# Performance work log

Measured on AMD Instinct MI355X. Metric: run time of the kernel, lower is better.

The kernel has to match this reference:

```python
import jax, jax.numpy as jnp
import numpy as np

G = 16  # grid (window) size, fixed in the module


def _ln_channels(x, w, b, eps=1e-5):
    # LayerNorm4D: normalize over channel dim of NCHW
    mu = x.mean(axis=1, keepdims=True)
    var = ((x - mu) ** 2).mean(axis=1, keepdims=True)
    return (x - mu) / jnp.sqrt(var + eps) * w[None, :, None, None] + b[None, :, None, None]


def setup_inputs() -> dict:
    key = jax.random.key(0)
    ks = jax.random.split(key, 8)
    B, C, H, W = 8, 256, 128, 128
    C8, F = C // 8, 4 * C
    s = 0.02
    return {
        "x": jax.random.normal(ks[0], (B, C, H, W), jnp.float32),
        "Wq": jax.random.normal(ks[1], (C8, C), jnp.float32) * s,
        "Wk": jax.random.normal(ks[2], (C8, C), jnp.float32) * s,
        "Wv": jax.random.normal(ks[3], (C, C), jnp.float32) * s,
        "gamma": jnp.float32(1.0),
        "W1": jax.random.normal(ks[4], (F, C), jnp.float32) * s,
        "b1": jnp.zeros((F,), jnp.float32),
        "W2": jax.random.normal(ks[5], (C, F), jnp.float32) * s,
        "b2": jnp.zeros((C,), jnp.float32),
        "ln1_w": jnp.ones((C,), jnp.float32),
        "ln1_b": jnp.zeros((C,), jnp.float32),
        "ln2_w": jnp.ones((C,), jnp.float32),
        "ln2_b": jnp.zeros((C,), jnp.float32),
    }


def reference(x, Wq, Wk, Wv, gamma, W1, b1, W2, b2, ln1_w, ln1_b, ln2_w, ln2_b):
    B, C, H, W = x.shape
    nh, nw = H // G, W // G
    N = G * G  # tokens per window
    # gather all 16x16 windows into the batch dim: [B*nh*nw, C, N]
    xw = x.reshape(B, C, nh, G, nw, G).transpose(0, 2, 4, 1, 3, 5).reshape(B * nh * nw, C, N)
    # SAGAN-style self-attention within each window
    q = jnp.einsum('oc,bcn->bno', Wq, xw)                 # [Bw, N, C/8]
    k = jnp.einsum('oc,bcn->bon', Wk, xw)                 # [Bw, C/8, N]
    attn = jax.nn.softmax(jnp.einsum('bno,bom->bnm', q, k), axis=-1)  # [Bw, N, N]
    v = jnp.einsum('oc,bcn->bon', Wv, xw)                 # [Bw, C, N]
    out = jnp.einsum('bcn,bmn->bcm', v, attn)             # v @ attn^T
    aw = gamma * out + xw
    # scatter windows back to NCHW
    xa = aw.reshape(B, nh, nw, C, G, G).transpose(0, 3, 1, 4, 2, 5).reshape(B, C, H, W)
    # FFN: 1x1 conv -> GELU(exact) -> 1x1 conv (dropout is identity in eval)
    h1 = jax.nn.gelu(jnp.einsum('fc,bchw->bfhw', W1, xa) + b1[None, :, None, None], approximate=False)
    y = jnp.einsum('cf,bfhw->bchw', W2, h1) + b2[None, :, None, None]
    x2 = xa + _ln_channels(y, ln1_w, ln1_b)
    return x2 + _ln_channels(x2, ln2_w, ln2_b)
```

## Files before the change

### kernel.cpp

```cpp
#include <hip/hip_runtime.h>
#include <hip/hip_bf16.h>

#define C_DIM 256
#define HW_DIM 16384
#define F_DIM 1024

typedef __hip_bfloat16 bf16;
typedef short short8 __attribute__((ext_vector_type(8)));
typedef float f32x4 __attribute__((ext_vector_type(4)));

__device__ __forceinline__ float bf2f(unsigned short u) {
  unsigned int x = ((unsigned int)u) << 16;
  return __uint_as_float(x);
}
__device__ __forceinline__ unsigned short f2bfbits(float v) {
  bf16 h = __float2bfloat16(v);
  return *(unsigned short*)&h;
}


__global__ __launch_bounds__(256) void prep_weights(
    const float* __restrict__ Wq, const float* __restrict__ Wk,
    const float* __restrict__ Wv, const float* __restrict__ W1,
    const float* __restrict__ W2, unsigned short* __restrict__ Wqkv,
    unsigned short* __restrict__ W1s, unsigned short* __restrict__ W2s) {
  int i = blockIdx.x * 256 + threadIdx.x;
  if (i < 320 * 256) {
    int r = i >> 8, c = i & 255;
    float v;
    if (r < 32)      v = Wq[r * 256 + c];
    else if (r < 64) v = Wk[(r - 32) * 256 + c];
    else             v = Wv[(r - 64) * 256 + c];
    Wqkv[i] = f2bfbits(v);
  }
  if (i < 32768) {
    int ft = i >> 9, ks = (i >> 6) & 7, l = i & 63;
    int f = ft * 16 + (l & 15), kb = ks * 32 + (l >> 4) * 8;
    #pragma unroll
    for (int j = 0; j < 8; ++j)
      W1s[i * 8 + j] = f2bfbits(W1[f * 256 + kb + j]);
  }
  if (i < 32768) {
    int ct = i >> 11, gks = (i >> 6) & 31, l = i & 63;
    int c = ct * 16 + (l & 15), fb = gks * 32 + (l >> 4) * 8;
    #pragma unroll
    for (int j = 0; j < 8; ++j)
      W2s[i * 8 + j] = f2bfbits(W2[c * 1024 + fb + j]);
  }
}

__global__ __launch_bounds__(256) void xprep_kernel(
    const float* __restrict__ x, unsigned short* __restrict__ Xfrag) {
  const int gtid = blockIdx.x * 256 + threadIdx.x;
  const int win = gtid >> 13;
  const int rem = gtid & 8191;
  const int mt = rem >> 9, ks = (rem >> 6) & 7, l = rem & 63;
  const int t = l & 15, q = l >> 4;
  const int b = win >> 6, wh = (win >> 3) & 7, ww = win & 7;
  const int h = wh * 16 + mt, w = ww * 16 + t;
  const int c0 = ks * 32 + q * 8;
  const float* xp = x + ((size_t)(b * 256 + c0) * 128 + h) * 128 + w;
  short8 v;
  #pragma unroll
  for (int j = 0; j < 8; ++j)
    v[j] = (short)f2bfbits(xp[(size_t)j * 16384]);
  *(short8*)(Xfrag + (size_t)gtid * 8) = v;
}

__global__ __launch_bounds__(256) void qkvproj_kernel(
    const unsigned short* __restrict__ Xfrag, const unsigned short* __restrict__ Wqkv,
    unsigned short* __restrict__ Qw, unsigned short* __restrict__ Kw,
    unsigned short* __restrict__ Vw) {
  const int bid = blockIdx.x;
  const int win = bid >> 2, mc = bid & 3;
  const int m0 = mc * 64;
  const int tid = threadIdx.x;
  const int wv = tid >> 6, l = tid & 63;
  const int t = l & 15, q = l >> 4;
  const unsigned short* Xb = Xfrag + (size_t)win * 65536;

  for (int mt = 0; mt < 4; ++mt) {
    short8 Bf[8];
    #pragma unroll
    for (int ks = 0; ks < 8; ++ks)
      Bf[ks] = *(const short8*)(Xb + (((size_t)(mc * 4 + mt) * 8 + ks) * 64 + l) * 8);
    #pragma unroll
    for (int rti = 0; rti < 5; ++rti) {
      const int rt = wv * 5 + rti;
      const int r0 = rt * 16;
      f32x4 acc = (f32x4){0.f, 0.f, 0.f, 0.f};
      #pragma unroll
      for (int ks = 0; ks < 8; ++ks) {
        short8 av = *(const short8*)(Wqkv + (size_t)(r0 + t) * 256 + ks * 32 + q * 8);
        acc = __builtin_amdgcn_mfma_f32_16x16x32_bf16(av, Bf[ks], acc, 0, 0, 0);
      }
      const int n = m0 + mt * 16 + t;
      if (rt < 4) {
        ushort4 u;
        u.x = f2bfbits(acc[0]); u.y = f2bfbits(acc[1]);
        u.z = f2bfbits(acc[2]); u.w = f2bfbits(acc[3]);
        unsigned short* dst = (rt < 2) ? Qw : Kw;
        int o0 = (rt & 1) * 16 + q * 4;
        *(ushort4*)(dst + ((size_t)win * 256 + n) * 32 + o0) = u;
      } else {
        #pragma unroll
        for (int r = 0; r < 4; ++r) {
          int c = r0 - 64 + q * 4 + r;
          Vw[((size_t)win * 256 + c) * 256 + n] = f2bfbits(acc[r]);
        }
      }
    }
  }
}

__global__ __launch_bounds__(256, 4) void attn_fused_kernel(
    const unsigned short* __restrict__ Qw, const unsigned short* __restrict__ Kw,
    const unsigned short* __restrict__ Vw, const unsigned short* __restrict__ Xfrag,
    const float* __restrict__ gamma, unsigned short* __restrict__ XAfrag) {
  __shared__ __align__(16) short Ps[2][64][72];
  __shared__ float Lpart[4][64];
  __shared__ float Ls[64];

  const int bid = blockIdx.x;
  const int wgb = (bid & 7) * 256 + (bid >> 3);
  const int win = wgb >> 2, wr = wgb & 3;

  const int tid = threadIdx.x;
  const int wc = tid >> 6, l = tid & 63;
  const int t = l & 15, q = l >> 4;

  f32x4 Oacc[4][4];
  #pragma unroll
  for (int k = 0; k < 4; ++k)
    #pragma unroll
    for (int i = 0; i < 4; ++i)
      Oacc[k][i] = (f32x4){0.f, 0.f, 0.f, 0.f};
  float lsum[16];
  #pragma unroll
  for (int e = 0; e < 16; ++e) lsum[e] = 0.f;

  const unsigned short* Qb = Qw + (size_t)win * 256 * 32;
  const unsigned short* Kb = Kw + (size_t)win * 256 * 32;
  const unsigned short* Vb = Vw + (size_t)win * 65536;

  short8 aq[4];
  #pragma unroll
  for (int i = 0; i < 4; ++i)
    aq[i] = *(const short8*)(Qb + (size_t)((wr * 4 + i) * 16 + t) * 32 + q * 8);

  for (int mcc = 0; mcc < 4; ++mcc) {
    const int buf = mcc & 1;
    {
      const int m0s = (mcc * 4 + wc) * 16;
      short8 bk = *(const short8*)(Kb + (size_t)(m0s + t) * 32 + q * 8);
      f32x4 sv[4];
      #pragma unroll
      for (int i = 0; i < 4; ++i)
        sv[i] = __builtin_amdgcn_mfma_f32_16x16x32_bf16(aq[i], bk, (f32x4){0.f,0.f,0.f,0.f}, 0, 0, 0);
      #pragma unroll
      for (int i = 0; i < 4; ++i) {
        #pragma unroll
        for (int r = 0; r < 4; ++r) {
          float e = __expf(sv[i][r]);
          lsum[i * 4 + r] += e;
          Ps[buf][i * 16 + q * 4 + r][wc * 16 + t] = (short)f2bfbits(e);
        }
      }
    }
    __syncthreads();
    #pragma unroll
    for (int ks2 = 0; ks2 < 2; ++ks2) {
      short8 ap[4], bv[4];
      #pragma unroll
      for (int i = 0; i < 4; ++i)
        ap[i] = *(const short8*)&Ps[buf][i * 16 + t][ks2 * 32 + q * 8];
      #pragma unroll
      for (int k = 0; k < 4; ++k)
        bv[k] = *(const short8*)(Vb + (size_t)((wc * 4 + k) * 16 + t) * 256 + mcc * 64 + ks2 * 32 + q * 8);
      #pragma unroll
      for (int k = 0; k < 4; ++k)
        #pragma unroll
        for (int i = 0; i < 4; ++i)
          Oacc[k][i] = __builtin_amdgcn_mfma_f32_16x16x32_bf16(bv[k], ap[i], Oacc[k][i], 0, 0, 0);
    }
  }

  #pragma unroll
  for (int mask = 1; mask < 16; mask <<= 1)
    #pragma unroll
    for (int e = 0; e < 16; ++e)
      lsum[e] += __shfl_xor(lsum[e], mask);
  __syncthreads();
  if (t == 0) {
    #pragma unroll
    for (int i = 0; i < 4; ++i)
      *(float4*)&Lpart[wc][i * 16 + q * 4] =
          make_float4(lsum[i * 4 + 0], lsum[i * 4 + 1], lsum[i * 4 + 2], lsum[i * 4 + 3]);
  }
  __syncthreads();
  if (tid < 64) {
    float s = Lpart[0][tid] + Lpart[1][tid] + Lpart[2][tid] + Lpart[3][tid];
    Ls[tid] = gamma[0] / s;
  }
  __syncthreads();

  const unsigned short* Xres = Xfrag + (size_t)win * 65536;
  unsigned short* XAb = XAfrag + (size_t)win * 65536;
  #pragma unroll
  for (int i = 0; i < 4; ++i) {
    const float ls = Ls[i * 16 + t];
    #pragma unroll
    for (int k = 0; k < 4; ++k) {
      const size_t off = (((size_t)(wr * 4 + i) * 8 + wc * 2 + (k >> 1)) * 64 +
                          ((k & 1) * 2 + (q >> 1)) * 16 + t) * 8 + (q & 1) * 4;
      ushort4 xa4 = *(const ushort4*)(Xres + off);
      const unsigned short* xp = (const unsigned short*)&xa4;
      ushort4 u;
      unsigned short* up = (unsigned short*)&u;
      #pragma unroll
      for (int r = 0; r < 4; ++r)
        up[r] = f2bfbits(ls * Oacc[k][i][r] + bf2f(xp[r]));
      *(ushort4*)(XAb + off) = u;
    }
  }
}

__global__ __launch_bounds__(256, 3) void ffn_mfma_kernel(
    const unsigned short* __restrict__ XAfrag,
    const unsigned short* __restrict__ W1s, const unsigned short* __restrict__ W2s,
    const float* __restrict__ b1, const float* __restrict__ b2,
    const float* __restrict__ ln1w, const float* __restrict__ ln1b,
    const float* __restrict__ ln2w, const float* __restrict__ ln2b,
    float* __restrict__ out) {
  __shared__ __align__(16) short Xf[4][8][64][8];
  __shared__ __align__(16) short Ht[64][136];
  __shared__ float red[2][4][64];

  const int bid = blockIdx.x;
  const int win = bid >> 2, mc = bid & 3;
  const int b = win >> 6, wh = (win >> 3) & 7, ww = win & 7;
  const int tid = threadIdx.x;
  const int wv = tid >> 6, l = tid & 63;
  const int p = l & 15, q = l >> 4;
  const unsigned short* XAb = XAfrag + (size_t)win * 65536 + (size_t)mc * 16384;

  {
    const short8* src = (const short8*)XAb;
    short8* dst = (short8*)&Xf[0][0][0][0];
    #pragma unroll
    for (int rep = 0; rep < 8; ++rep)
      dst[rep * 256 + tid] = src[rep * 256 + tid];
  }
  __syncthreads();

  f32x4 Yacc[4][4];
  #pragma unroll
  for (int i = 0; i < 4; ++i)
    #pragma unroll
    for (int pt = 0; pt < 4; ++pt)
      Yacc[i][pt] = (f32x4){0.f, 0.f, 0.f, 0.f};

  const short8* W1s8 = (const short8*)W1s;
  const short8* W2s8 = (const short8*)W2s;

  for (int fc = 0; fc < 8; ++fc) {
    f32x4 Hacc[2][4];
    #pragma unroll
    for (int i = 0; i < 2; ++i)
      #pragma unroll
      for (int pt = 0; pt < 4; ++pt)
        Hacc[i][pt] = (f32x4){0.f, 0.f, 0.f, 0.f};
    const int f0 = (fc * 8 + wv * 2) * 8;
    #pragma unroll
    for (int ks = 0; ks < 8; ++ks) {
      short8 a0 = W1s8[(f0 + ks) * 64 + l];
      short8 a1 = W1s8[(f0 + 8 + ks) * 64 + l];
      #pragma unroll
      for (int pt = 0; pt < 4; ++pt) {
        short8 bf = *(const short8*)&Xf[pt][ks][l][0];
        Hacc[0][pt] = __builtin_amdgcn_mfma_f32_16x16x32_bf16(a0, bf, Hacc[0][pt], 0, 0, 0);
        Hacc[1][pt] = __builtin_amdgcn_mfma_f32_16x16x32_bf16(a1, bf, Hacc[1][pt], 0, 0, 0);
      }
    }
    __syncthreads();
    #pragma unroll
    for (int i = 0; i < 2; ++i) {
      float4 bv1 = *(const float4*)(b1 + fc * 128 + wv * 32 + i * 16 + q * 4);
      #pragma unroll
      for (int pt = 0; pt < 4; ++pt) {
        ushort4 hbv;
        unsigned short* hp = (unsigned short*)&hbv;
        #pragma unroll
        for (int r = 0; r < 4; ++r) {
          float v = Hacc[i][pt][r] + ((const float*)&bv1)[r];
          float u = 0.7978845608f * fmaf(0.044715f * v, v * v, v);
          float e = __expf(2.f * u);
          float g = v - v / (e + 1.f);
          hp[r] = f2bfbits(g);
        }
        *(ushort4*)&Ht[pt * 16 + p][wv * 32 + i * 16 + q * 4] = hbv;
      }
    }
    __syncthreads();
    #pragma unroll
    for (int fs = 0; fs < 4; ++fs) {
      short8 av[4];
      #pragma unroll
      for (int i = 0; i < 4; ++i)
        av[i] = W2s8[((wv * 4 + i) * 32 + fc * 4 + fs) * 64 + l];
      #pragma unroll
      for (int pt = 0; pt < 4; ++pt) {
        short8 bf = *(const short8*)&Ht[pt * 16 + p][fs * 32 + q * 8];
        #pragma unroll
        for (int i = 0; i < 4; ++i)
          Yacc[i][pt] = __builtin_amdgcn_mfma_f32_16x16x32_bf16(av[i], bf, Yacc[i][pt], 0, 0, 0);
      }
    }
  }

  #pragma unroll
  for (int i = 0; i < 4; ++i) {
    float4 bb = *(const float4*)(b2 + wv * 64 + i * 16 + q * 4);
    #pragma unroll
    for (int pt = 0; pt < 4; ++pt)
      #pragma unroll
      for (int r = 0; r < 4; ++r)
        Yacc[i][pt][r] += ((const float*)&bb)[r];
  }

  #pragma unroll
  for (int pt = 0; pt < 4; ++pt) {
    float ss = 0.f, sq = 0.f;
    #pragma unroll
    for (int i = 0; i < 4; ++i)
      #pragma unroll
      for (int r = 0; r < 4; ++r) { float v = Yacc[i][pt][r]; ss += v; sq += v * v; }
    ss += __shfl_xor(ss, 16); sq += __shfl_xor(sq, 16);
    ss += __shfl_xor(ss, 32); sq += __shfl_xor(sq, 32);
    if (l < 16) { red[0][wv][pt * 16 + l] = ss; red[1][wv][pt * 16 + l] = sq; }
  }
  __syncthreads();
  if (tid < 64) {
    float S  = red[0][0][tid] + red[0][1][tid] + red[0][2][tid] + red[0][3][tid];
    float Q2 = red[1][0][tid] + red[1][1][tid] + red[1][2][tid] + red[1][3][tid];
    float m = S * 0.00390625f;
    float va = Q2 * 0.00390625f - m * m;
    red[0][0][tid] = m; red[1][0][tid] = rsqrtf(va + 1e-5f);
  }
  __syncthreads();
  #pragma unroll
  for (int i = 0; i < 4; ++i) {
    float4 w1v = *(const float4*)(ln1w + wv * 64 + i * 16 + q * 4);
    float4 b1v = *(const float4*)(ln1b + wv * 64 + i * 16 + q * 4);
    const int ksx = wv * 2 + (i >> 1);
    const int lq = (i & 1) * 2 + (q >> 1);
    #pragma unroll
    for (int pt = 0; pt < 4; ++pt) {
      int px = pt * 16 + p;
      float mu = red[0][0][px], rs = red[1][0][px];
      ushort4 xa4 = *(const ushort4*)&Xf[pt][ksx][lq * 16 + p][(q & 1) * 4];
      const unsigned short* xp = (const unsigned short*)&xa4;
      #pragma unroll
      for (int r = 0; r < 4; ++r)
        Yacc[i][pt][r] = bf2f(xp[r]) + (Yacc[i][pt][r] - mu) * rs * ((const float*)&w1v)[r] + ((const float*)&b1v)[r];
    }
  }
  __syncthreads();
  #pragma unroll
  for (int pt = 0; pt < 4; ++pt) {
    float ss = 0.f, sq = 0.f;
    #pragma unroll
    for (int i = 0; i < 4; ++i)
      #pragma unroll
      for (int r = 0; r < 4; ++r) { float v = Yacc[i][pt][r]; ss += v; sq += v * v; }
    ss += __shfl_xor(ss, 16); sq += __shfl_xor(sq, 16);
    ss += __shfl_xor(ss, 32); sq += __shfl_xor(sq, 32);
    if (l < 16) { red[0][wv][pt * 16 + l] = ss; red[1][wv][pt * 16 + l] = sq; }
  }
  __syncthreads();
  if (tid < 64) {
    float S  = red[0][0][tid] + red[0][1][tid] + red[0][2][tid] + red[0][3][tid];
    float Q2 = red[1][0][tid] + red[1][1][tid] + red[1][2][tid] + red[1][3][tid];
    float m = S * 0.00390625f;
    float va = Q2 * 0.00390625f - m * m;
    red[0][0][tid] = m; red[1][0][tid] = rsqrtf(va + 1e-5f);
  }
  __syncthreads();
  #pragma unroll
  for (int i = 0; i < 4; ++i) {
    float4 w2v = *(const float4*)(ln2w + wv * 64 + i * 16 + q * 4);
    float4 b2v = *(const float4*)(ln2b + wv * 64 + i * 16 + q * 4);
    #pragma unroll
    for (int pt = 0; pt < 4; ++pt) {
      int px = pt * 16 + p;
      float mu = red[0][0][px], rs = red[1][0][px];
      #pragma unroll
      for (int r = 0; r < 4; ++r) {
        int c = wv * 64 + i * 16 + q * 4 + r;
        float x2 = Yacc[i][pt][r];
        float o = x2 + (x2 - mu) * rs * ((const float*)&w2v)[r] + ((const float*)&b2v)[r];
        out[(((size_t)(b * 256 + c) * 128) + wh * 16 + mc * 4 + pt) * 128 + ww * 16 + p] = o;
      }
    }
  }
}

extern "C" void kernel_launch(void* const* d_in, const int* in_sizes, int n_in,
                              void* d_out, int out_size, void* d_ws, size_t ws_size,
                              hipStream_t stream) {
  const float* x     = (const float*)d_in[0];
  const float* Wq    = (const float*)d_in[1];
  const float* Wk    = (const float*)d_in[2];
  const float* Wv    = (const float*)d_in[3];
  const float* gamma = (const float*)d_in[4];
  const float* W1    = (const float*)d_in[5];
  const float* b1    = (const float*)d_in[6];
  const float* W2    = (const float*)d_in[7];
  const float* b2    = (const float*)d_in[8];
  const float* ln1w  = (const float*)d_in[9];
  const float* ln1b  = (const float*)d_in[10];
  const float* ln2w  = (const float*)d_in[11];
  const float* ln2b  = (const float*)d_in[12];
  float* out = (float*)d_out;

  char* wsb = (char*)d_ws;
  unsigned short* XAfrag = (unsigned short*)wsb;
  unsigned short* Vw     = (unsigned short*)(wsb + 67108864);
  unsigned short* Xfrag  = (unsigned short*)(wsb + 134217728);
  unsigned short* Qw     = (unsigned short*)(wsb + 201326592);
  unsigned short* Kw     = (unsigned short*)(wsb + 209715200);
  unsigned short* Wqkv   = (unsigned short*)(wsb + 218103808);
  unsigned short* W1s    = (unsigned short*)(wsb + 218267648);
  unsigned short* W2s    = (unsigned short*)(wsb + 218791936);

  prep_weights<<<1024, 256, 0, stream>>>(Wq, Wk, Wv, W1, W2, Wqkv, W1s, W2s);
  xprep_kernel<<<16384, 256, 0, stream>>>(x, Xfrag);
  qkvproj_kernel<<<2048, 256, 0, stream>>>(Xfrag, Wqkv, Qw, Kw, Vw);
  attn_fused_kernel<<<2048, 256, 0, stream>>>(Qw, Kw, Vw, Xfrag, gamma, XAfrag);
  ffn_mfma_kernel<<<2048, 256, 0, stream>>>(XAfrag, W1s, W2s, b1, b2, ln1w, ln1b, ln2w, ln2b, out);
}
```

Before: 671.5 us.

## Fuse x-prep into QKV projection and attention into FFN kernel

Merges the x conversion kernel into the QKV projection, which now stages the bf16 x fragments in shared memory while still writing them out for the residual. Merges attention and FFN so the attention output (XA) stays in shared memory instead of round-tripping through a 64MB workspace buffer, and aliases LDS buffers to fit. The GELU division becomes a hardware reciprocal. This removes two launches and large global writes and reads, but lowers the attention occupancy hint from 4 to 3 and lengthens per-block serial work.

```diff
diff --git a/kernel.cpp b/kernel.cpp
--- a/kernel.cpp
+++ b/kernel.cpp
@@ -49,41 +49,45 @@
   }
 }
 
-__global__ __launch_bounds__(256) void xprep_kernel(
-    const float* __restrict__ x, unsigned short* __restrict__ Xfrag) {
-  const int gtid = blockIdx.x * 256 + threadIdx.x;
-  const int win = gtid >> 13;
-  const int rem = gtid & 8191;
-  const int mt = rem >> 9, ks = (rem >> 6) & 7, l = rem & 63;
-  const int t = l & 15, q = l >> 4;
-  const int b = win >> 6, wh = (win >> 3) & 7, ww = win & 7;
-  const int h = wh * 16 + mt, w = ww * 16 + t;
-  const int c0 = ks * 32 + q * 8;
-  const float* xp = x + ((size_t)(b * 256 + c0) * 128 + h) * 128 + w;
-  short8 v;
-  #pragma unroll
-  for (int j = 0; j < 8; ++j)
-    v[j] = (short)f2bfbits(xp[(size_t)j * 16384]);
-  *(short8*)(Xfrag + (size_t)gtid * 8) = v;
-}
-
-__global__ __launch_bounds__(256) void qkvproj_kernel(
-    const unsigned short* __restrict__ Xfrag, const unsigned short* __restrict__ Wqkv,
-    unsigned short* __restrict__ Qw, unsigned short* __restrict__ Kw,
-    unsigned short* __restrict__ Vw) {
+__global__ __launch_bounds__(256) void qkvx_kernel(
+    const float* __restrict__ x, const unsigned short* __restrict__ Wqkv,
+    unsigned short* __restrict__ Xfrag, unsigned short* __restrict__ Qw,
+    unsigned short* __restrict__ Kw, unsigned short* __restrict__ Vw) {
+  __shared__ __align__(16) short Xs[4][8][64][8];
+
   const int bid = blockIdx.x;
   const int win = bid >> 2, mc = bid & 3;
+  const int b = win >> 6, wh = (win >> 3) & 7, ww = win & 7;
   const int m0 = mc * 64;
   const int tid = threadIdx.x;
   const int wv = tid >> 6, l = tid & 63;
   const int t = l & 15, q = l >> 4;
-  const unsigned short* Xb = Xfrag + (size_t)win * 65536;
+
+  unsigned short* XFb = Xfrag + (size_t)win * 65536 + (size_t)mc * 16384;
+  short8* XsLin = (short8*)&Xs[0][0][0][0];
+
+  #pragma unroll
+  for (int rep = 0; rep < 8; ++rep) {
+    const int idx = rep * 256 + tid;
+    const int mt_l = idx >> 9, kss = (idx >> 6) & 7, ll = idx & 63;
+    const int tt = ll & 15, qq = ll >> 4;
+    const int h = wh * 16 + mc * 4 + mt_l, w = ww * 16 + tt;
+    const int c0 = kss * 32 + qq * 8;
+    const float* xp = x + ((size_t)(b * 256 + c0) * 128 + h) * 128 + w;
+    short8 v;
+    #pragma unroll
+    for (int j = 0; j < 8; ++j)
+      v[j] = (short)f2bfbits(xp[(size_t)j * 16384]);
+    XsLin[idx] = v;
+    *(short8*)(XFb + (size_t)idx * 8) = v;
+  }
+  __syncthreads();
 
   for (int mt = 0; mt < 4; ++mt) {
     short8 Bf[8];
     #pragma unroll
     for (int ks = 0; ks < 8; ++ks)
-      Bf[ks] = *(const short8*)(Xb + (((size_t)(mc * 4 + mt) * 8 + ks) * 64 + l) * 8);
+      Bf[ks] = *(const short8*)&Xs[mt][ks][l][0];
     #pragma unroll
     for (int rti = 0; rti < 5; ++rti) {
       const int rt = wv * 5 + rti;
@@ -113,17 +117,28 @@
   }
 }
 
-__global__ __launch_bounds__(256, 4) void attn_fused_kernel(
+__global__ __launch_bounds__(256, 3) void attn_ffn_kernel(
     const unsigned short* __restrict__ Qw, const unsigned short* __restrict__ Kw,
     const unsigned short* __restrict__ Vw, const unsigned short* __restrict__ Xfrag,
-    const float* __restrict__ gamma, unsigned short* __restrict__ XAfrag) {
-  __shared__ __align__(16) short Ps[2][64][72];
-  __shared__ float Lpart[4][64];
+    const float* __restrict__ gamma,
+    const unsigned short* __restrict__ W1s, const unsigned short* __restrict__ W2s,
+    const float* __restrict__ b1, const float* __restrict__ b2,
+    const float* __restrict__ ln1w, const float* __restrict__ ln1b,
+    const float* __restrict__ ln2w, const float* __restrict__ ln2b,
+    float* __restrict__ out) {
+  __shared__ __align__(16) short XfPs[16384];
+  __shared__ __align__(16) short Ht[64][136];
+  __shared__ float red[2][4][64];
   __shared__ float Ls[64];
+
+  short (*Ps)[64][72] = (short(*)[64][72])&XfPs[0];
+  float* Lpart = (float*)&XfPs[9216];
+  short (*Xf)[8][64][8] = (short(*)[8][64][8])&XfPs[0];
 
   const int bid = blockIdx.x;
   const int wgb = (bid & 7) * 256 + (bid >> 3);
   const int win = wgb >> 2, wr = wgb & 3;
+  const int b = win >> 6, wh = (win >> 3) & 7, ww = win & 7;
 
   const int tid = threadIdx.x;
   const int wc = tid >> 6, l = tid & 63;
@@ -194,64 +209,40 @@
   if (t == 0) {
     #pragma unroll
     for (int i = 0; i < 4; ++i)
-      *(float4*)&Lpart[wc][i * 16 + q * 4] =
+      *(float4*)&Lpart[wc * 64 + i * 16 + q * 4] =
           make_float4(lsum[i * 4 + 0], lsum[i * 4 + 1], lsum[i * 4 + 2], lsum[i * 4 + 3]);
   }
   __syncthreads();
   if (tid < 64) {
-    float s = Lpart[0][tid] + Lpart[1][tid] + Lpart[2][tid] + Lpart[3][tid];
+    float s = Lpart[tid] + Lpart[64 + tid] + Lpart[128 + tid] + Lpart[192 + tid];
     Ls[tid] = gamma[0] / s;
   }
   __syncthreads();
 
   const unsigned short* Xres = Xfrag + (size_t)win * 65536;
-  unsigned short* XAb = XAfrag + (size_t)win * 65536;
   #pragma unroll
   for (int i = 0; i < 4; ++i) {
     const float ls = Ls[i * 16 + t];
     #pragma unroll
     for (int k = 0; k < 4; ++k) {
-      const size_t off = (((size_t)(wr * 4 + i) * 8 + wc * 2 + (k >> 1)) * 64 +
-                          ((k & 1) * 2 + (q >> 1)) * 16 + t) * 8 + (q & 1) * 4;
-      ushort4 xa4 = *(const ushort4*)(Xres + off);
+      const int ksx = wc * 2 + (k >> 1);
+      const int lx = ((k & 1) * 2 + (q >> 1)) * 16 + t;
+      const int jx = (q & 1) * 4;
+      const size_t goff = (((size_t)(wr * 4 + i) * 8 + ksx) * 64 + lx) * 8 + jx;
+      ushort4 xa4 = *(const ushort4*)(Xres + goff);
       const unsigned short* xp = (const unsigned short*)&xa4;
       ushort4 u;
       unsigned short* up = (unsigned short*)&u;
       #pragma unroll
       for (int r = 0; r < 4; ++r)
         up[r] = f2bfbits(ls * Oacc[k][i][r] + bf2f(xp[r]));
-      *(ushort4*)(XAb + off) = u;
-    }
-  }
-}
-
-__global__ __launch_bounds__(256, 3) void ffn_mfma_kernel(
-    const unsigned short* __restrict__ XAfrag,
-    const unsigned short* __restrict__ W1s, const unsigned short* __restrict__ W2s,
-    const float* __restrict__ b1, const float* __restrict__ b2,
-    const float* __restrict__ ln1w, const float* __restrict__ ln1b,
-    const float* __restrict__ ln2w, const float* __restrict__ ln2b,
-    float* __restrict__ out) {
-  __shared__ __align__(16) short Xf[4][8][64][8];
-  __shared__ __align__(16) short Ht[64][136];
-  __shared__ float red[2][4][64];
-
-  const int bid = blockIdx.x;
-  const int win = bid >> 2, mc = bid & 3;
-  const int b = win >> 6, wh = (win >> 3) & 7, ww = win & 7;
-  const int tid = threadIdx.x;
-  const int wv = tid >> 6, l = tid & 63;
-  const int p = l & 15, q = l >> 4;
-  const unsigned short* XAb = XAfrag + (size_t)win * 65536 + (size_t)mc * 16384;
-
-  {
-    const short8* src = (const short8*)XAb;
-    short8* dst = (short8*)&Xf[0][0][0][0];
-    #pragma unroll
-    for (int rep = 0; rep < 8; ++rep)
-      dst[rep * 256 + tid] = src[rep * 256 + tid];
-  }
-  __syncthreads();
+      *(ushort4*)&Xf[i][ksx][lx][jx] = u;
+    }
+  }
+  __syncthreads();
+
+  const int p = t;
+  const int wv = wc;
 
   f32x4 Yacc[4][4];
   #pragma unroll
@@ -295,7 +286,7 @@
           float v = Hacc[i][pt][r] + ((const float*)&bv1)[r];
           float u = 0.7978845608f * fmaf(0.044715f * v, v * v, v);
           float e = __expf(2.f * u);
-          float g = v - v / (e + 1.f);
+          float g = v - v * __builtin_amdgcn_rcpf(e + 1.f);
           hp[r] = f2bfbits(g);
         }
         *(ushort4*)&Ht[pt * 16 + p][wv * 32 + i * 16 + q * 4] = hbv;
@@ -399,7 +390,7 @@
         int c = wv * 64 + i * 16 + q * 4 + r;
         float x2 = Yacc[i][pt][r];
         float o = x2 + (x2 - mu) * rs * ((const float*)&w2v)[r] + ((const float*)&b2v)[r];
-        out[(((size_t)(b * 256 + c) * 128) + wh * 16 + mc * 4 + pt) * 128 + ww * 16 + p] = o;
+        out[(((size_t)(b * 256 + c) * 128) + wh * 16 + wr * 4 + pt) * 128 + ww * 16 + p] = o;
       }
     }
   }
@@ -424,18 +415,16 @@
   float* out = (float*)d_out;
 
   char* wsb = (char*)d_ws;
-  unsigned short* XAfrag = (unsigned short*)wsb;
-  unsigned short* Vw     = (unsigned short*)(wsb + 67108864);
-  unsigned short* Xfrag  = (unsigned short*)(wsb + 134217728);
-  unsigned short* Qw     = (unsigned short*)(wsb + 201326592);
-  unsigned short* Kw     = (unsigned short*)(wsb + 209715200);
-  unsigned short* Wqkv   = (unsigned short*)(wsb + 218103808);
-  unsigned short* W1s    = (unsigned short*)(wsb + 218267648);
-  unsigned short* W2s    = (unsigned short*)(wsb + 218791936);
+  unsigned short* Xfrag = (unsigned short*)wsb;
+  unsigned short* Vw    = (unsigned short*)(wsb + 67108864);
+  unsigned short* Qw    = (unsigned short*)(wsb + 134217728);
+  unsigned short* Kw    = (unsigned short*)(wsb + 142606336);
+  unsigned short* Wqkv  = (unsigned short*)(wsb + 150994944);
+  unsigned short* W1s   = (unsigned short*)(wsb + 151158784);
+  unsigned short* W2s   = (unsigned short*)(wsb + 151683072);
 
   prep_weights<<<1024, 256, 0, stream>>>(Wq, Wk, Wv, W1, W2, Wqkv, W1s, W2s);
-  xprep_kernel<<<16384, 256, 0, stream>>>(x, Xfrag);
-  qkvproj_kernel<<<2048, 256, 0, stream>>>(Xfrag, Wqkv, Qw, Kw, Vw);
-  attn_fused_kernel<<<2048, 256, 0, stream>>>(Qw, Kw, Vw, Xfrag, gamma, XAfrag);
-  ffn_mfma_kernel<<<2048, 256, 0, stream>>>(XAfrag, W1s, W2s, b1, b2, ln1w, ln1b, ln2w, ln2b, out);
-}
+  qkvx_kernel<<<2048, 256, 0, stream>>>(x, Wqkv, Xfrag, Qw, Kw, Vw);
+  attn_ffn_kernel<<<2048, 256, 0, stream>>>(Qw, Kw, Vw, Xfrag, gamma,
+                                            W1s, W2s, b1, b2, ln1w, ln1b, ln2w, ln2b, out);
+}
```

New measurement: 580.9 us. 1.16x faster.
